# Performance work log

Measured on AMD Instinct MI355X. Metric: run time of the kernel, lower is better.

## Reference

```python
import jax, jax.numpy as jnp
import numpy as np

EPS = 1e-6

def _rmsnorm(x, w):
    # RMSNorm in float32 as in the torch module, then rescale by weight
    xf = x.astype(jnp.float32)
    y = xf * jax.lax.rsqrt(jnp.mean(xf * xf, axis=-1, keepdims=True) + EPS)
    return y.astype(x.dtype) * w

def setup_inputs() -> dict:
    key = jax.random.key(0)
    k0, k1, k2 = jax.random.split(key, 3)
    B, T, C = 2, 1024, 256
    x = jax.random.normal(k0, (B, T, C), jnp.float32)
    w_qkv = jax.random.normal(k1, (3 * C, C), jnp.float32) / np.float32(np.sqrt(C))
    w_proj = jax.random.normal(k2, (C, C), jnp.float32) / np.float32(np.sqrt(C))
    qn_w = jnp.ones((2,), jnp.float32)
    kn_w = jnp.ones((2,), jnp.float32)
    return {"x": x, "w_qkv": w_qkv, "w_proj": w_proj, "qn_w": qn_w, "kn_w": kn_w}

def reference(x, w_qkv, w_proj, qn_w, kn_w):
    B, T, C = x.shape
    HD = 2                      # head_dim forced to 2 by GPTConfig invariant
    H = C // HD                 # n_head = n_embd // 2
    qkv = x @ w_qkv.T           # (B, T, 3C); Linear has bias=False
    q, k, v = jnp.split(qkv, 3, axis=-1)
    heads = lambda t: t.reshape(B, T, H, HD).transpose(0, 2, 1, 3)  # (B,H,T,2)
    q = _rmsnorm(heads(q), qn_w)
    k = _rmsnorm(heads(k), kn_w)
    v = heads(v)
    scale = np.float32(1.0 / np.sqrt(HD))
    att = jnp.einsum('bhtd,bhsd->bhts', q, k) * scale   # (B,H,T,T)
    causal = jnp.tril(jnp.ones((T, T), bool))
    att = jnp.where(causal, att, jnp.float32(-1e30))
    att = jax.nn.softmax(att, axis=-1)
    y = jnp.einsum('bhts,bhsd->bhtd', att, v)           # (B,H,T,2)
    y = y.transpose(0, 2, 1, 3).reshape(B, T, C)
    return y @ w_proj.T
```

## Files before the change

### kernel.cpp

```cpp
#include <hip/hip_runtime.h>

#define T_SEQ   1024
#define C_DIM   256
#define H_HEADS 128
#define NTOK    2048
#define BH      256
#define NBLK    768

#define MAGIC1  0x1357ACE5u
#define MAGIC2  0x2468BD17u

typedef unsigned short u16;
typedef unsigned int   u32;
typedef __attribute__((ext_vector_type(8))) short bf16x8;
typedef __attribute__((ext_vector_type(4))) float f32x4;
typedef __attribute__((ext_vector_type(2))) float f32x2;
typedef __attribute__((ext_vector_type(2))) unsigned int u32x2;

__device__ __forceinline__ float bf2f(u16 u) {
  return __uint_as_float(((u32)u) << 16);
}
__device__ __forceinline__ u16 f2bf(float f) {
  u32 u = __float_as_uint(f);
  u32 r = u + 0x7fffu + ((u >> 16) & 1u);
  return (u16)(r >> 16);
}

__device__ __forceinline__ void stwt2(void* p, f32x2 v) {
  asm volatile("global_store_dwordx2 %0, %1, off sc0 sc1" :: "v"(p), "v"(v) : "memory");
}
__device__ __forceinline__ void stwt2u(void* p, u32x2 v) {
  asm volatile("global_store_dwordx2 %0, %1, off sc0 sc1" :: "v"(p), "v"(v) : "memory");
}

__device__ __forceinline__ bf16x8 ldsf(const u16* plane, int row, int kk) {
  int off = (row * 128 + kk * 2) ^ ((row & 7) << 4);
  return *(const bf16x8*)((const char*)plane + off);
}
__device__ __forceinline__ void cvt_store(float4 g, u16* hp, int lo_u16,
                                          int r, int c4) {
  ushort4 h4, l4;
  h4.x = f2bf(g.x); l4.x = f2bf(g.x - bf2f(h4.x));
  h4.y = f2bf(g.y); l4.y = f2bf(g.y - bf2f(h4.y));
  h4.z = f2bf(g.z); l4.z = f2bf(g.z - bf2f(h4.z));
  h4.w = f2bf(g.w); l4.w = f2bf(g.w - bf2f(h4.w));
  int off = (r * 128 + c4 * 2) ^ ((r & 7) << 4);
  *(ushort4*)((char*)hp + off) = h4;
  *(ushort4*)((char*)(hp + lo_u16) + off) = l4;
}

#define AG __HIP_MEMORY_SCOPE_AGENT
__device__ __forceinline__ void slot_set(u32* s, u32 v) {
  __hip_atomic_store(s, v, __ATOMIC_RELAXED, AG);
}
__device__ __forceinline__ u32 slot_get(const u32* s) {
  return __hip_atomic_load(s, __ATOMIC_RELAXED, AG);
}

__device__ __forceinline__ void attn_unit(
    char* smem, const float* __restrict__ q, const float* __restrict__ kk,
    const float* __restrict__ vv, u32* __restrict__ yP,
    int head, int g, bool stage, int tid, int lane, int w)
{
  float4* skA = (float4*)smem;
  float4* skB = (float4*)(smem + 8192);
  float (*red)[256][3] = (float (*)[256][3])(smem + 16384);

  const int qb = g * 256;
  const int S  = qb + 256;

  if (stage) {
    const float4* kh = (const float4*)(kk + head * (T_SEQ * 2));
    const float4* vh = (const float4*)(vv + head * (T_SEQ * 2));
    for (int i = tid; i < (S >> 1); i += 256) {
      float4 k4 = kh[i];
      float4 v4 = vh[i];
      skA[i] = make_float4(k4.x, k4.z, k4.y, k4.w);
      skB[i] = make_float4(v4.x, v4.z, v4.y, v4.w);
    }
  }

  const float LS = 0.70710678118f * 1.44269504089f;
  f32x2 qxb[4], qyb[4];
  int   tq[4];
#pragma unroll
  for (int j = 0; j < 4; ++j) {
    int t = qb + j * 64 + lane;
    tq[j] = t;
    float2 qv = *(const float2*)&q[(head * T_SEQ + t) * 2];
    float sx = qv.x * LS, sy = qv.y * LS;
    qxb[j] = (f32x2){sx, sx};
    qyb[j] = (f32x2){sy, sy};
  }
  __syncthreads();

  f32x2 denp[4] = {}, nxp[4] = {}, nyp[4] = {};

  const int cbp = qb >> 3;
  const int p0 = w * cbp, p1 = p0 + cbp;
#pragma unroll 2
  for (int p = p0; p < p1; ++p) {
    float4 A = skA[p], V = skB[p];
    f32x2 kx = {A.x, A.y}, ky = {A.z, A.w};
    f32x2 vx = {V.x, V.y}, vy = {V.z, V.w};
#pragma unroll
    for (int j = 0; j < 4; ++j) {
      f32x2 sp = __builtin_elementwise_fma(qxb[j], kx, qyb[j] * ky);
      f32x2 ep = { __builtin_amdgcn_exp2f(sp.x), __builtin_amdgcn_exp2f(sp.y) };
      denp[j] += ep;
      nxp[j] = __builtin_elementwise_fma(ep, vx, nxp[j]);
      nyp[j] = __builtin_elementwise_fma(ep, vy, nyp[j]);
    }
  }
  const int dp0 = (qb >> 1) + w * 32;
#pragma unroll 2
  for (int p = dp0; p < dp0 + 32; ++p) {
    float4 A = skA[p], V = skB[p];
    f32x2 kx = {A.x, A.y}, ky = {A.z, A.w};
    f32x2 vx = {V.x, V.y}, vy = {V.z, V.w};
    const int s0 = 2 * p;
#pragma unroll
    for (int j = 0; j < 4; ++j) {
      f32x2 sp = __builtin_elementwise_fma(qxb[j], kx, qyb[j] * ky);
      f32x2 ep = { __builtin_amdgcn_exp2f(sp.x), __builtin_amdgcn_exp2f(sp.y) };
      ep.x = (s0     <= tq[j]) ? ep.x : 0.f;
      ep.y = (s0 + 1 <= tq[j]) ? ep.y : 0.f;
      denp[j] += ep;
      nxp[j] = __builtin_elementwise_fma(ep, vx, nxp[j]);
      nyp[j] = __builtin_elementwise_fma(ep, vy, nyp[j]);
    }
  }

#pragma unroll
  for (int j = 0; j < 4; ++j) {
    red[w][j * 64 + lane][0] = denp[j].x + denp[j].y;
    red[w][j * 64 + lane][1] = nxp[j].x + nxp[j].y;
    red[w][j * 64 + lane][2] = nyp[j].x + nyp[j].y;
  }
  __syncthreads();

  float dd = 0.f, ax = 0.f, ay = 0.f;
#pragma unroll
  for (int ww = 0; ww < 4; ++ww) {
    dd += red[ww][tid][0];
    ax += red[ww][tid][1];
    ay += red[ww][tid][2];
  }
  float inv = 1.f / dd;
  float ox = ax * inv, oy = ay * inv;
  u32 hx = f2bf(ox), hy = f2bf(oy);
  float rx = ox - bf2f((u16)hx), ry = oy - bf2f((u16)hy);
  u32x2 e = { hx | (hy << 16), (u32)f2bf(rx) | ((u32)f2bf(ry) << 16) };
  stwt2u(yP + ((size_t)head * T_SEQ + qb + tid) * 2, e);
}

__global__ __launch_bounds__(256, 3) void k_fused(
    const float* __restrict__ x, const float* __restrict__ wqkv,
    const float* __restrict__ wproj,
    const float* __restrict__ qnw, const float* __restrict__ knw,
    float* __restrict__ out,
    u32* __restrict__ slots1,
    u32* __restrict__ slotsY,
    float* __restrict__ q, float* __restrict__ kk, float* __restrict__ vv,
    u32* __restrict__ yP)
{
  __shared__ __align__(16) char smem[28672];

  const int tid  = threadIdx.x;
  const int blk  = blockIdx.x;
  const int lane = tid & 63;
  const int w    = tid >> 6;

  {
    u16* L = (u16*)smem;
    const int bx   = blk & 63, by = blk >> 6;
    const int row0 = bx * 32, col0 = by * 64;
    const int fr   = lane & 15;
    const int ko   = (lane >> 4) * 8;

    f32x4 acc[2] = {};
    float4 rx[2], rw[4];

    auto LOADR = [&](int kc) {
#pragma unroll
      for (int it = 0; it < 2; ++it) {
        int idx = it * 256 + tid;
        rx[it] = *(const float4*)&x[(row0 + (idx >> 4)) * C_DIM + kc * 64 + (idx & 15) * 4];
      }
#pragma unroll
      for (int it = 0; it < 4; ++it) {
        int idx = it * 256 + tid;
        rw[it] = *(const float4*)&wqkv[(col0 + (idx >> 4)) * C_DIM + kc * 64 + (idx & 15) * 4];
      }
    };

    LOADR(0);
    for (int kc = 0; kc < 4; ++kc) {
#pragma unroll
      for (int it = 0; it < 2; ++it) {
        int idx = it * 256 + tid;
        cvt_store(rx[it], L, 2048, idx >> 4, (idx & 15) * 4);
      }
#pragma unroll
      for (int it = 0; it < 4; ++it) {
        int idx = it * 256 + tid;
        cvt_store(rw[it], L + 4096, 4096, idx >> 4, (idx & 15) * 4);
      }
      __syncthreads();
      if (kc < 3) LOADR(kc + 1);
#pragma unroll
      for (int ks = 0; ks < 2; ++ks) {
        const int kk2 = ks * 32 + ko;
        bf16x8 bhi = ldsf(L + 4096, w * 16 + fr, kk2);
        bf16x8 blo = ldsf(L + 8192, w * 16 + fr, kk2);
#pragma unroll
        for (int rt = 0; rt < 2; ++rt) {
          bf16x8 ahi = ldsf(L,        rt * 16 + fr, kk2);
          bf16x8 alo = ldsf(L + 2048, rt * 16 + fr, kk2);
          acc[rt] = __builtin_amdgcn_mfma_f32_16x16x32_bf16(alo, bhi, acc[rt], 0, 0, 0);
          acc[rt] = __builtin_amdgcn_mfma_f32_16x16x32_bf16(ahi, blo, acc[rt], 0, 0, 0);
          acc[rt] = __builtin_amdgcn_mfma_f32_16x16x32_bf16(ahi, bhi, acc[rt], 0, 0, 0);
        }
      }
      __syncthreads();
    }

    const int sec = col0 >> 8;
    const int cg  = col0 + w * 16 + fr;
    const int d   = cg & 1;
    const float wn = (sec == 0) ? qnw[d] : (sec == 1) ? knw[d] : 1.f;
    float* sf = (float*)smem;
    const int cl = w * 16 + fr;

#pragma unroll
    for (int rt = 0; rt < 2; ++rt) {
#pragma unroll
      for (int i = 0; i < 4; ++i) {
        float val = acc[rt][i];
        if (sec < 2) {
          float pv = __shfl_xor(val, 1);
          float rr = rsqrtf(0.5f * (val * val + pv * pv) + 1e-6f);
          val = val * rr * wn;
        }
        int tl = rt * 16 + (lane >> 4) * 4 + i;
        sf[tl * 66 + cl] = val;
      }
    }
    __syncthreads();

    float* dst = (sec == 0) ? q : (sec == 1) ? kk : vv;
    const int b  = row0 >> 10, t0 = row0 & 1023;
    const int h0 = (col0 & 255) >> 1;
#pragma unroll
    for (int it = 0; it < 4; ++it) {
      int seg = w * 8 + it * 2 + (lane >> 5);
      int w2  = lane & 31;
      f32x2 v2 = { sf[w2 * 66 + seg * 2], sf[w2 * 66 + seg * 2 + 1] };
      stwt2(dst + ((size_t)((b * H_HEADS + h0 + seg)) * T_SEQ + t0 + w2) * 2, v2);
    }
  }

  asm volatile("s_waitcnt vmcnt(0)" ::: "memory");
  __syncthreads();
  if (tid == 0) slot_set(slots1 + blk, MAGIC1);

  {
    const int head = blk & 255;
    const int b    = head >> 7;
    const int hq   = (head & 127) >> 5;
    const int b4   = b * 4;
    const int h    = head & 127;
    const int g1st = (blk < 256) ? 3 : (blk < 512) ? 2 : 1;
    const int kvn  = 8 * (g1st + 1);
    const int qlo  = (blk >= 512) ? 0 : g1st * 8;
    const int qn   = (blk >= 512) ? 16 : 8;

    if (w == 0) {
      int guard = 0;
      for (;;) {
        bool ok = true;
        if (lane < 32) {
          if (lane < kvn) {
            int bxk = b * 32 + lane;
            ok &= (slot_get(slots1 + (4 + hq) * 64 + bxk) == MAGIC1);
            ok &= (slot_get(slots1 + (8 + hq) * 64 + bxk) == MAGIC1);
          }
        } else if (lane - 32 < qn) {
          int bxq = b * 32 + qlo + (lane - 32);
          ok &= (slot_get(slots1 + hq * 64 + bxq) == MAGIC1);
        }
        if (__all(ok)) break;
        __builtin_amdgcn_s_sleep(8);
        if (++guard > (1 << 20)) break;
      }
    }
    __builtin_amdgcn_fence(__ATOMIC_ACQUIRE, "workgroup");
    __syncthreads();

    attn_unit(smem, q, kk, vv, yP, head, g1st, true, tid, lane, w);
    asm volatile("s_waitcnt vmcnt(0)" ::: "memory");
    __syncthreads();
    if (tid == 0) slot_set(slotsY + (b4 + g1st) * 128 + h, MAGIC2);

    if (blk >= 512) {
      attn_unit(smem, q, kk, vv, yP, head, 0, false, tid, lane, w);
      asm volatile("s_waitcnt vmcnt(0)" ::: "memory");
      __syncthreads();
      if (tid == 0) slot_set(slotsY + (b4 + 0) * 128 + h, MAGIC2);
    }
  }

  if (blk >= 256) {
    const int blkp = blk - 256;
    u16* L = (u16*)smem;
    const int bx   = blkp & 63, by = blkp >> 6;
    const int row0 = bx * 32, col0 = by * 32;
    const int b    = row0 >> 10, t0 = row0 & 1023;
    const int gs   = t0 >> 8;
    const int fr   = lane & 15;
    const int ko   = (lane >> 4) * 8;
    const int ar   = (w >> 1) * 16 + fr;
    const int br   = (w & 1) * 16 + fr;
    const int tl_  = tid & 31, hb = tid >> 5;

    f32x4 acc = {};
    float4 rw[2];
    u32x2  ry[4];

    auto LOADW = [&](int kc) {
#pragma unroll
      for (int it = 0; it < 2; ++it) {
        int idx = it * 256 + tid;
        rw[it] = *(const float4*)&wproj[(col0 + (idx >> 4)) * C_DIM + kc * 64 + (idx & 15) * 4];
      }
    };
    auto LOADY = [&](int kc) {
#pragma unroll
      for (int j = 0; j < 4; ++j) {
        int h = hb * 4 + j;
        ry[j] = *(const u32x2*)(yP + ((size_t)(b * H_HEADS + kc * 32 + h) * T_SEQ + t0 + tl_) * 2);
      }
    };

    LOADW(0);
    if (w == 0) {
      const u32* sy = slotsY + (b * 4 + gs) * 128;
      int guard = 0;
      for (;;) {
        bool ok = (slot_get(sy + lane) == MAGIC2) &
                  (slot_get(sy + 64 + lane) == MAGIC2);
        if (__all(ok)) break;
        __builtin_amdgcn_s_sleep(8);
        if (++guard > (1 << 20)) break;
      }
    }
    __builtin_amdgcn_fence(__ATOMIC_ACQUIRE, "workgroup");
    __syncthreads();

    LOADY(0);
    for (int kc = 0; kc < 4; ++kc) {
#pragma unroll
      for (int j = 0; j < 4; ++j) {
        int h = hb * 4 + j;
        int off = (tl_ * 128 + h * 4) ^ ((tl_ & 7) << 4);
        *(u32*)((char*)L + off)        = ry[j].x;
        *(u32*)((char*)L + 4096 + off) = ry[j].y;
      }
#pragma unroll
      for (int it = 0; it < 2; ++it) {
        int idx = it * 256 + tid;
        cvt_store(rw[it], L + 4096, 2048, idx >> 4, (idx & 15) * 4);
      }
      __syncthreads();
      if (kc < 3) { LOADW(kc + 1); LOADY(kc + 1); }
#pragma unroll
      for (int ks = 0; ks < 2; ++ks) {
        const int kk2 = ks * 32 + ko;
        bf16x8 bhi = ldsf(L + 4096, br, kk2);
        bf16x8 blo = ldsf(L + 6144, br, kk2);
        bf16x8 ahi = ldsf(L,        ar, kk2);
        bf16x8 alo = ldsf(L + 2048, ar, kk2);
        acc = __builtin_amdgcn_mfma_f32_16x16x32_bf16(alo, bhi, acc, 0, 0, 0);
        acc = __builtin_amdgcn_mfma_f32_16x16x32_bf16(ahi, blo, acc, 0, 0, 0);
        acc = __builtin_amdgcn_mfma_f32_16x16x32_bf16(ahi, bhi, acc, 0, 0, 0);
      }
      __syncthreads();
    }

    const int cg = col0 + (w & 1) * 16 + fr;
#pragma unroll
    for (int i = 0; i < 4; ++i) {
      int n = row0 + (w >> 1) * 16 + (lane >> 4) * 4 + i;
      out[n * C_DIM + cg] = acc[i];
    }
  }
}

extern "C" void kernel_launch(void* const* d_in, const int* in_sizes, int n_in,
                              void* d_out, int out_size, void* d_ws, size_t ws_size,
                              hipStream_t stream) {
  const float* x     = (const float*)d_in[0];
  const float* wqkv  = (const float*)d_in[1];
  const float* wproj = (const float*)d_in[2];
  const float* qnw   = (const float*)d_in[3];
  const float* knw   = (const float*)d_in[4];

  char* p = (char*)d_ws;
  u32* slots1 = (u32*)p;  p += 768 * 4;
  u32* slotsY = (u32*)p;  p += 1024 * 4;
  p = (char*)d_ws + 8192;
  float* q  = (float*)p;  p += (size_t)BH * T_SEQ * 2 * 4;
  float* kk = (float*)p;  p += (size_t)BH * T_SEQ * 2 * 4;
  float* vv = (float*)p;  p += (size_t)BH * T_SEQ * 2 * 4;
  u32* yP  = (u32*)p;     p += (size_t)BH * T_SEQ * 2 * 4;

  k_fused<<<NBLK, 256, 0, stream>>>(x, wqkv, wproj, qnw, knw, (float*)d_out,
                                    slots1, slotsY, q, kk, vv, yP);
}
```

Measured before the change: 111.5 us.

## Split attention into one query-group per block across 1024 blocks

Grid grows from 768 to 1024 blocks so each block handles exactly one attention query group (g=0..3 per head) instead of some blocks doing two. The extra 256 blocks do only attention for g=3, and the QKV GEMM and projection phases are restricted to the first 768 blocks. Launch bounds rise to 4 blocks per SU/CU, and the inner key loops are manually unrolled by 4 with batched LDS loads. This is meant to balance causal-attention work and raise occupancy, at the cost of more register pressure and more blocks spinning on cross-block slots.

```diff
diff --git a/kernel.cpp b/kernel.cpp
--- a/kernel.cpp
+++ b/kernel.cpp
@@ -5,7 +5,7 @@
 #define H_HEADS 128
 #define NTOK    2048
 #define BH      256
-#define NBLK    768
+#define NBLK    1024
 
 #define MAGIC1  0x1357ACE5u
 #define MAGIC2  0x2468BD17u
@@ -60,7 +60,7 @@
 __device__ __forceinline__ void attn_unit(
     char* smem, const float* __restrict__ q, const float* __restrict__ kk,
     const float* __restrict__ vv, u32* __restrict__ yP,
-    int head, int g, bool stage, int tid, int lane, int w)
+    int head, int g, int tid, int lane, int w)
 {
   float4* skA = (float4*)smem;
   float4* skB = (float4*)(smem + 8192);
@@ -69,7 +69,7 @@
   const int qb = g * 256;
   const int S  = qb + 256;
 
-  if (stage) {
+  {
     const float4* kh = (const float4*)(kk + head * (T_SEQ * 2));
     const float4* vh = (const float4*)(vv + head * (T_SEQ * 2));
     for (int i = tid; i < (S >> 1); i += 256) {
@@ -98,36 +98,50 @@
 
   const int cbp = qb >> 3;
   const int p0 = w * cbp, p1 = p0 + cbp;
-#pragma unroll 2
-  for (int p = p0; p < p1; ++p) {
-    float4 A = skA[p], V = skB[p];
-    f32x2 kx = {A.x, A.y}, ky = {A.z, A.w};
-    f32x2 vx = {V.x, V.y}, vy = {V.z, V.w};
-#pragma unroll
-    for (int j = 0; j < 4; ++j) {
-      f32x2 sp = __builtin_elementwise_fma(qxb[j], kx, qyb[j] * ky);
-      f32x2 ep = { __builtin_amdgcn_exp2f(sp.x), __builtin_amdgcn_exp2f(sp.y) };
-      denp[j] += ep;
-      nxp[j] = __builtin_elementwise_fma(ep, vx, nxp[j]);
-      nyp[j] = __builtin_elementwise_fma(ep, vy, nyp[j]);
+  for (int p = p0; p < p1; p += 4) {
+    float4 A0 = skA[p],     V0 = skB[p];
+    float4 A1 = skA[p + 1], V1 = skB[p + 1];
+    float4 A2 = skA[p + 2], V2 = skB[p + 2];
+    float4 A3 = skA[p + 3], V3 = skB[p + 3];
+#pragma unroll
+    for (int u = 0; u < 4; ++u) {
+      float4 A = (u == 0) ? A0 : (u == 1) ? A1 : (u == 2) ? A2 : A3;
+      float4 V = (u == 0) ? V0 : (u == 1) ? V1 : (u == 2) ? V2 : V3;
+      f32x2 kx = {A.x, A.y}, ky = {A.z, A.w};
+      f32x2 vx = {V.x, V.y}, vy = {V.z, V.w};
+#pragma unroll
+      for (int j = 0; j < 4; ++j) {
+        f32x2 sp = __builtin_elementwise_fma(qxb[j], kx, qyb[j] * ky);
+        f32x2 ep = { __builtin_amdgcn_exp2f(sp.x), __builtin_amdgcn_exp2f(sp.y) };
+        denp[j] += ep;
+        nxp[j] = __builtin_elementwise_fma(ep, vx, nxp[j]);
+        nyp[j] = __builtin_elementwise_fma(ep, vy, nyp[j]);
+      }
     }
   }
   const int dp0 = (qb >> 1) + w * 32;
-#pragma unroll 2
-  for (int p = dp0; p < dp0 + 32; ++p) {
-    float4 A = skA[p], V = skB[p];
-    f32x2 kx = {A.x, A.y}, ky = {A.z, A.w};
-    f32x2 vx = {V.x, V.y}, vy = {V.z, V.w};
-    const int s0 = 2 * p;
-#pragma unroll
-    for (int j = 0; j < 4; ++j) {
-      f32x2 sp = __builtin_elementwise_fma(qxb[j], kx, qyb[j] * ky);
-      f32x2 ep = { __builtin_amdgcn_exp2f(sp.x), __builtin_amdgcn_exp2f(sp.y) };
-      ep.x = (s0     <= tq[j]) ? ep.x : 0.f;
-      ep.y = (s0 + 1 <= tq[j]) ? ep.y : 0.f;
-      denp[j] += ep;
-      nxp[j] = __builtin_elementwise_fma(ep, vx, nxp[j]);
-      nyp[j] = __builtin_elementwise_fma(ep, vy, nyp[j]);
+  for (int p = dp0; p < dp0 + 32; p += 4) {
+    float4 A0 = skA[p],     V0 = skB[p];
+    float4 A1 = skA[p + 1], V1 = skB[p + 1];
+    float4 A2 = skA[p + 2], V2 = skB[p + 2];
+    float4 A3 = skA[p + 3], V3 = skB[p + 3];
+#pragma unroll
+    for (int u = 0; u < 4; ++u) {
+      float4 A = (u == 0) ? A0 : (u == 1) ? A1 : (u == 2) ? A2 : A3;
+      float4 V = (u == 0) ? V0 : (u == 1) ? V1 : (u == 2) ? V2 : V3;
+      f32x2 kx = {A.x, A.y}, ky = {A.z, A.w};
+      f32x2 vx = {V.x, V.y}, vy = {V.z, V.w};
+      const int s0 = 2 * (p + u);
+#pragma unroll
+      for (int j = 0; j < 4; ++j) {
+        f32x2 sp = __builtin_elementwise_fma(qxb[j], kx, qyb[j] * ky);
+        f32x2 ep = { __builtin_amdgcn_exp2f(sp.x), __builtin_amdgcn_exp2f(sp.y) };
+        ep.x = (s0     <= tq[j]) ? ep.x : 0.f;
+        ep.y = (s0 + 1 <= tq[j]) ? ep.y : 0.f;
+        denp[j] += ep;
+        nxp[j] = __builtin_elementwise_fma(ep, vx, nxp[j]);
+        nyp[j] = __builtin_elementwise_fma(ep, vy, nyp[j]);
+      }
     }
   }
 
@@ -154,7 +168,7 @@
   stwt2u(yP + ((size_t)head * T_SEQ + qb + tid) * 2, e);
 }
 
-__global__ __launch_bounds__(256, 3) void k_fused(
+__global__ __launch_bounds__(256, 4) void k_fused(
     const float* __restrict__ x, const float* __restrict__ wqkv,
     const float* __restrict__ wproj,
     const float* __restrict__ qnw, const float* __restrict__ knw,
@@ -171,7 +185,7 @@
   const int lane = tid & 63;
   const int w    = tid >> 6;
 
-  {
+  if (blk < 768) {
     u16* L = (u16*)smem;
     const int bx   = blk & 63, by = blk >> 6;
     const int row0 = bx * 32, col0 = by * 64;
@@ -258,22 +272,24 @@
       f32x2 v2 = { sf[w2 * 66 + seg * 2], sf[w2 * 66 + seg * 2 + 1] };
       stwt2(dst + ((size_t)((b * H_HEADS + h0 + seg)) * T_SEQ + t0 + w2) * 2, v2);
     }
-  }
-
-  asm volatile("s_waitcnt vmcnt(0)" ::: "memory");
-  __syncthreads();
-  if (tid == 0) slot_set(slots1 + blk, MAGIC1);
+
+    asm volatile("s_waitcnt vmcnt(0)" ::: "memory");
+    __syncthreads();
+    if (tid == 0) slot_set(slots1 + blk, MAGIC1);
+  }
 
   {
-    const int head = blk & 255;
-    const int b    = head >> 7;
-    const int hq   = (head & 127) >> 5;
-    const int b4   = b * 4;
-    const int h    = head & 127;
-    const int g1st = (blk < 256) ? 3 : (blk < 512) ? 2 : 1;
-    const int kvn  = 8 * (g1st + 1);
-    const int qlo  = (blk >= 512) ? 0 : g1st * 8;
-    const int qn   = (blk >= 512) ? 16 : 8;
+    int g, head;
+    if (blk >= 768)      { g = 3; head = blk - 768; }
+    else if (blk < 256)  { g = 2; head = blk; }
+    else if (blk < 512)  { g = 1; head = blk - 256; }
+    else                 { g = 0; head = blk - 512; }
+
+    const int b   = head >> 7;
+    const int hq  = (head & 127) >> 5;
+    const int h   = head & 127;
+    const int kvn = 8 * (g + 1);
+    const int qlo = g * 8;
 
     if (w == 0) {
       int guard = 0;
@@ -285,7 +301,7 @@
             ok &= (slot_get(slots1 + (4 + hq) * 64 + bxk) == MAGIC1);
             ok &= (slot_get(slots1 + (8 + hq) * 64 + bxk) == MAGIC1);
           }
-        } else if (lane - 32 < qn) {
+        } else if (lane - 32 < 8) {
           int bxq = b * 32 + qlo + (lane - 32);
           ok &= (slot_get(slots1 + hq * 64 + bxq) == MAGIC1);
         }
@@ -297,20 +313,13 @@
     __builtin_amdgcn_fence(__ATOMIC_ACQUIRE, "workgroup");
     __syncthreads();
 
-    attn_unit(smem, q, kk, vv, yP, head, g1st, true, tid, lane, w);
+    attn_unit(smem, q, kk, vv, yP, head, g, tid, lane, w);
     asm volatile("s_waitcnt vmcnt(0)" ::: "memory");
     __syncthreads();
-    if (tid == 0) slot_set(slotsY + (b4 + g1st) * 128 + h, MAGIC2);
-
-    if (blk >= 512) {
-      attn_unit(smem, q, kk, vv, yP, head, 0, false, tid, lane, w);
-      asm volatile("s_waitcnt vmcnt(0)" ::: "memory");
-      __syncthreads();
-      if (tid == 0) slot_set(slotsY + (b4 + 0) * 128 + h, MAGIC2);
-    }
-  }
-
-  if (blk >= 256) {
+    if (tid == 0) slot_set(slotsY + (b * 4 + g) * 128 + h, MAGIC2);
+  }
+
+  if (blk >= 256 && blk < 768) {
     const int blkp = blk - 256;
     u16* L = (u16*)smem;
     const int bx   = blkp & 63, by = blkp >> 6;
```

Measured after the change: 110.4 us. Within noise of the previous version (-1.0%).
